# Optimization experiments

Measured on AMD Instinct MI355X. Metric: run time of the kernel, lower is better.

Reference implementation:

```python
import jax, jax.numpy as jnp
import numpy as np

B, H, S, DK = 4, 16, 1024, 64


def setup_inputs() -> dict:
    key = jax.random.key(0)
    kq, kk, kv, km = jax.random.split(key, 4)
    q = jax.random.normal(kq, (B, H, S, DK), dtype=jnp.float32)
    k = jax.random.normal(kk, (B, H, S, DK), dtype=jnp.float32)
    v = jax.random.normal(kv, (B, H, S, DK), dtype=jnp.float32)
    mask = jax.random.randint(km, (B, 1, 1, S), 0, 2).astype(jnp.int32)
    return {"q": q, "k": k, "v": v, "mask": mask}


def reference(q, k, v, mask):
    dk = q.shape[-1]
    scale = 1.0 / np.sqrt(dk).astype(np.float32)
    # [B,H,S,S] scores
    qk = jnp.einsum("bhqd,bhkd->bhqk", q, k) * scale
    qk = jnp.where(mask == 0, jnp.float32(-10000.0), qk)
    attn_weight = jax.nn.softmax(qk, axis=-1)
    # NOTE: faithful to source bug — uses raw masked scores qk, not attn_weight
    output = jnp.einsum("bhqk,bhkd->bhqd", qk, v)
    return (output, attn_weight)
```

## Files before the change

kernel.cpp:

```cpp
#include <hip/hip_runtime.h>


typedef __attribute__((ext_vector_type(4))) float floatx4;
typedef __attribute__((ext_vector_type(8))) short shortx8;
typedef __attribute__((ext_vector_type(8))) unsigned short ushortx8;
typedef __attribute__((ext_vector_type(4))) int intx4;

#define S_ 1024
#define D_ 64
#define NELEM_ 4194304
#define ATTN_OFF 4194304
#define SCN 1040

__device__ __forceinline__ unsigned short f32_to_bf16(float f) {
    union { float f; unsigned u; } a; a.f = f;
    unsigned u = a.u;
    u += 0x7fffu + ((u >> 16) & 1u);
    return (unsigned short)(u >> 16);
}

__device__ __forceinline__ float bf16_to_f32(unsigned short h) {
    union { unsigned u; float f; } a; a.u = ((unsigned)h) << 16;
    return a.f;
}

__device__ __forceinline__ ushortx8 pack8u(floatx4 a, floatx4 b) {
    ushortx8 r;
    r[0] = f32_to_bf16(a[0]); r[1] = f32_to_bf16(a[1]);
    r[2] = f32_to_bf16(a[2]); r[3] = f32_to_bf16(a[3]);
    r[4] = f32_to_bf16(b[0]); r[5] = f32_to_bf16(b[1]);
    r[6] = f32_to_bf16(b[2]); r[7] = f32_to_bf16(b[3]);
    return r;
}

__global__ __launch_bounds__(256) void pack_kv(const float* __restrict__ k,
                                               const float* __restrict__ v,
                                               unsigned short* __restrict__ kbt,
                                               unsigned short* __restrict__ vtp) {
    __shared__ float tile[64][65];
    if (blockIdx.x < 1024) {
        int g = blockIdx.x * 256 + threadIdx.x;
        int lane = g & 63;
        int kt   = (g >> 6) & 63;
        int bh   = g >> 12;
        int quad = lane >> 4;
        int l15  = lane & 15;
        const float* src = k + ((size_t)(bh * S_ + kt * 16 + l15)) * D_ + quad * 8;
        floatx4 f0 = *(const floatx4*)(src);
        floatx4 f1 = *(const floatx4*)(src + 4);
        floatx4 f2 = *(const floatx4*)(src + 32);
        floatx4 f3 = *(const floatx4*)(src + 36);
        unsigned short* dst = kbt + (size_t)g * 16;
        *(ushortx8*)(dst)     = pack8u(f0, f1);
        *(ushortx8*)(dst + 8) = pack8u(f2, f3);
    } else {
        int blk = blockIdx.x - 1024;
        int bh = blk >> 4;
        int s0 = (blk & 15) << 6;
        int tid = threadIdx.x;
        int r  = tid >> 2;
        int c0 = (tid & 3) << 4;
        const float* src = v + ((size_t)(bh * S_ + s0 + r)) * D_ + c0;
        #pragma unroll
        for (int j = 0; j < 4; ++j) {
            floatx4 f = *(const floatx4*)(src + j * 4);
            tile[r][c0 + j*4 + 0] = f[0];
            tile[r][c0 + j*4 + 1] = f[1];
            tile[r][c0 + j*4 + 2] = f[2];
            tile[r][c0 + j*4 + 3] = f[3];
        }
        __syncthreads();
        int d  = tid >> 2;
        int so = (tid & 3) << 4;
        int dt  = d >> 4;
        int l15 = d & 15;
        ushortx8 h0, h1;
        #pragma unroll
        for (int j = 0; j < 8; ++j) h0[j] = f32_to_bf16(tile[so + j][d]);
        #pragma unroll
        for (int j = 0; j < 8; ++j) h1[j] = f32_to_bf16(tile[so + 8 + j][d]);
        int sA = s0 + so;
        int ksA = sA >> 5, qA = (sA & 31) >> 3;
        int sB = sA + 8;
        int ksB = sB >> 5, qB = (sB & 31) >> 3;
        size_t baseA = ((((size_t)bh * 4 + dt) * 32 + ksA) * 64 + qA * 16 + l15) * 8;
        size_t baseB = ((((size_t)bh * 4 + dt) * 32 + ksB) * 64 + qB * 16 + l15) * 8;
        *(ushortx8*)(vtp + baseA) = h0;
        *(ushortx8*)(vtp + baseB) = h1;
    }
}

__global__ __launch_bounds__(256, 4) void attn_main(
    const float* __restrict__ q,
    const int* __restrict__ mask,
    const unsigned short* __restrict__ KbT,
    const unsigned short* __restrict__ VtP,
    float* __restrict__ out)
{
    __shared__ unsigned short sc[16 * SCN];
    __shared__ int msk[1024];

    int g   = blockIdx.x;
    int xcd = g & 7;
    int i   = g >> 3;
    int bh  = xcd * 8 + (i >> 6);
    int q0  = (i & 63) << 4;
    int b   = bh >> 4;
    int tid = threadIdx.x;

    ((intx4*)msk)[tid] = ((const intx4*)(mask + (b << 10)))[tid];

    int w    = tid >> 6;
    int lane = tid & 63;
    int l15  = lane & 15;
    int quad = lane >> 4;

    shortx8 qf0, qf1;
    {
        const float* qb = q + ((size_t)(bh * S_ + q0 + l15)) * D_ + quad * 8;
        floatx4 a0 = *(const floatx4*)(qb);
        floatx4 a1 = *(const floatx4*)(qb + 4);
        floatx4 b0 = *(const floatx4*)(qb + 32);
        floatx4 b1 = *(const floatx4*)(qb + 36);
        ushortx8 u0 = pack8u(a0, a1);
        ushortx8 u1 = pack8u(b0, b1);
        qf0 = (shortx8)u0;
        qf1 = (shortx8)u1;
    }

    __syncthreads();

    {
        const unsigned short* kb = KbT + ((size_t)bh * 64 * 64 + lane) * 16;
        for (int kt = w; kt < 64; kt += 4) {
            const unsigned short* p = kb + (size_t)kt * (64 * 16);
            shortx8 kf0 = *(const shortx8*)(p);
            shortx8 kf1 = *(const shortx8*)(p + 8);
            floatx4 acc = {0.f, 0.f, 0.f, 0.f};
            acc = __builtin_amdgcn_mfma_f32_16x16x32_bf16(qf0, kf0, acc, 0, 0, 0);
            acc = __builtin_amdgcn_mfma_f32_16x16x32_bf16(qf1, kf1, acc, 0, 0, 0);
            int n0 = kt << 4;
            int mv = msk[n0 + l15];
            int col = n0 + l15;
            #pragma unroll
            for (int r = 0; r < 4; ++r) {
                unsigned short h = mv ? f32_to_bf16(acc[r] * 0.125f)
                                      : (unsigned short)0xC61C;
                sc[(quad * 4 + r) * SCN + col] = h;
            }
        }
    }
    __syncthreads();

    {
        float* attnb = out + ATTN_OFF + ((size_t)(bh * S_ + q0)) * S_;
        for (int rr = 0; rr < 4; ++rr) {
            int row = (w << 2) + rr;
            const unsigned short* srow = sc + row * SCN;
            float vv[16];
            #pragma unroll
            for (int c = 0; c < 2; ++c) {
                ushortx8 h = *(const ushortx8*)(srow + (c << 9) + lane * 8);
                #pragma unroll
                for (int j = 0; j < 8; ++j) vv[c * 8 + j] = bf16_to_f32(h[j]);
            }
            float m = vv[0];
            #pragma unroll
            for (int j = 1; j < 16; ++j) m = fmaxf(m, vv[j]);
            #pragma unroll
            for (int off = 32; off; off >>= 1) m = fmaxf(m, __shfl_xor(m, off));
            float s = 0.f;
            #pragma unroll
            for (int j = 0; j < 16; ++j) { vv[j] = __expf(vv[j] - m); s += vv[j]; }
            #pragma unroll
            for (int off = 32; off; off >>= 1) s += __shfl_xor(s, off);
            float inv = 1.0f / s;
            float* arow = attnb + (size_t)row * S_ + lane * 8;
            #pragma unroll
            for (int c = 0; c < 2; ++c) {
                floatx4 o0 = { vv[c*8+0]*inv, vv[c*8+1]*inv, vv[c*8+2]*inv, vv[c*8+3]*inv };
                floatx4 o1 = { vv[c*8+4]*inv, vv[c*8+5]*inv, vv[c*8+6]*inv, vv[c*8+7]*inv };
                *(floatx4*)(arow + (c << 9))     = o0;
                *(floatx4*)(arow + (c << 9) + 4) = o1;
            }
        }
    }

    {
        const unsigned short* vb = VtP + (((size_t)bh * 4 + w) * 32) * (64 * 8) + lane * 8;
        const unsigned short* sr = sc + l15 * SCN + quad * 8;
        floatx4 oacc = {0.f, 0.f, 0.f, 0.f};
        #pragma unroll 4
        for (int ks = 0; ks < 32; ++ks) {
            shortx8 af = *(const shortx8*)(sr + (ks << 5));
            shortx8 bf = *(const shortx8*)(vb + (ks << 9));
            oacc = __builtin_amdgcn_mfma_f32_16x16x32_bf16(af, bf, oacc, 0, 0, 0);
        }
        int d0 = w << 4;
        float* ob = out + ((size_t)(bh * S_ + q0 + (quad << 2))) * D_ + d0 + l15;
        #pragma unroll
        for (int r = 0; r < 4; ++r) ob[(size_t)r * D_] = oacc[r];
    }
}

extern "C" void kernel_launch(void* const* d_in, const int* in_sizes, int n_in,
                              void* d_out, int out_size, void* d_ws, size_t ws_size,
                              hipStream_t stream) {
    const float* q   = (const float*)d_in[0];
    const float* k   = (const float*)d_in[1];
    const float* v   = (const float*)d_in[2];
    const int* mask  = (const int*)d_in[3];
    float* out = (float*)d_out;
    unsigned short* KbT = (unsigned short*)d_ws;
    unsigned short* VtP = KbT + NELEM_;
    pack_kv<<<2048, 256, 0, stream>>>(k, v, KbT, VtP);
    attn_main<<<4096, 256, 0, stream>>>(q, mask, KbT, VtP, out);
}
```

Before: 378.3 us.

## Use 1024-thread blocks over 64 query rows with 2D wave split

Each block now covers 64 query rows with 16 waves split into 4 row groups and 4 column groups. This reuses K and V tiles across more rows per block and cuts the grid to 1024 blocks. Odd waves run the PV matmul before the softmax write-out and even waves do the reverse, so MFMA and store traffic overlap. The cost is about 133 KB of LDS per block and the removal of the XCD-aware block swizzle, which limits blocks per CU and may hurt L2 locality.

```diff
diff --git a/kernel.cpp b/kernel.cpp
--- a/kernel.cpp
+++ b/kernel.cpp
@@ -90,34 +90,34 @@
     }
 }
 
-__global__ __launch_bounds__(256, 4) void attn_main(
+__global__ __launch_bounds__(1024, 4) void attn_main(
     const float* __restrict__ q,
     const int* __restrict__ mask,
     const unsigned short* __restrict__ KbT,
     const unsigned short* __restrict__ VtP,
     float* __restrict__ out)
 {
-    __shared__ unsigned short sc[16 * SCN];
+    __shared__ unsigned short sc[64 * SCN];
     __shared__ int msk[1024];
 
-    int g   = blockIdx.x;
-    int xcd = g & 7;
-    int i   = g >> 3;
-    int bh  = xcd * 8 + (i >> 6);
-    int q0  = (i & 63) << 4;
+    int blk = blockIdx.x;
+    int bh  = blk >> 4;
+    int q0  = (blk & 15) << 6;
     int b   = bh >> 4;
     int tid = threadIdx.x;
 
-    ((intx4*)msk)[tid] = ((const intx4*)(mask + (b << 10)))[tid];
+    msk[tid] = mask[(b << 10) + tid];
 
     int w    = tid >> 6;
     int lane = tid & 63;
     int l15  = lane & 15;
     int quad = lane >> 4;
+    int rg   = w & 3;
+    int cg   = w >> 2;
 
     shortx8 qf0, qf1;
     {
-        const float* qb = q + ((size_t)(bh * S_ + q0 + l15)) * D_ + quad * 8;
+        const float* qb = q + ((size_t)(bh * S_ + q0 + rg * 16 + l15)) * D_ + quad * 8;
         floatx4 a0 = *(const floatx4*)(qb);
         floatx4 a1 = *(const floatx4*)(qb + 4);
         floatx4 b0 = *(const floatx4*)(qb + 32);
@@ -132,7 +132,9 @@
 
     {
         const unsigned short* kb = KbT + ((size_t)bh * 64 * 64 + lane) * 16;
-        for (int kt = w; kt < 64; kt += 4) {
+        #pragma unroll 4
+        for (int t = 0; t < 16; ++t) {
+            int kt = (cg << 4) + t;
             const unsigned short* p = kb + (size_t)kt * (64 * 16);
             shortx8 kf0 = *(const shortx8*)(p);
             shortx8 kf1 = *(const shortx8*)(p + 8);
@@ -146,13 +148,13 @@
             for (int r = 0; r < 4; ++r) {
                 unsigned short h = mv ? f32_to_bf16(acc[r] * 0.125f)
                                       : (unsigned short)0xC61C;
-                sc[(quad * 4 + r) * SCN + col] = h;
+                sc[(rg * 16 + quad * 4 + r) * SCN + col] = h;
             }
         }
     }
     __syncthreads();
 
-    {
+    auto phase2 = [&]() {
         float* attnb = out + ATTN_OFF + ((size_t)(bh * S_ + q0)) * S_;
         for (int rr = 0; rr < 4; ++rr) {
             int row = (w << 2) + rr;
@@ -184,11 +186,10 @@
                 *(floatx4*)(arow + (c << 9) + 4) = o1;
             }
         }
-    }
-
-    {
-        const unsigned short* vb = VtP + (((size_t)bh * 4 + w) * 32) * (64 * 8) + lane * 8;
-        const unsigned short* sr = sc + l15 * SCN + quad * 8;
+    };
+    auto phase3 = [&]() {
+        const unsigned short* vb = VtP + (((size_t)bh * 4 + cg) * 32) * (64 * 8) + lane * 8;
+        const unsigned short* sr = sc + (rg * 16 + l15) * SCN + quad * 8;
         floatx4 oacc = {0.f, 0.f, 0.f, 0.f};
         #pragma unroll 4
         for (int ks = 0; ks < 32; ++ks) {
@@ -196,11 +197,13 @@
             shortx8 bf = *(const shortx8*)(vb + (ks << 9));
             oacc = __builtin_amdgcn_mfma_f32_16x16x32_bf16(af, bf, oacc, 0, 0, 0);
         }
-        int d0 = w << 4;
-        float* ob = out + ((size_t)(bh * S_ + q0 + (quad << 2))) * D_ + d0 + l15;
+        float* ob = out + ((size_t)(bh * S_ + q0 + rg * 16 + (quad << 2))) * D_
+                        + (cg << 4) + l15;
         #pragma unroll
         for (int r = 0; r < 4; ++r) ob[(size_t)r * D_] = oacc[r];
-    }
+    };
+    if (w & 1) { phase3(); phase2(); }
+    else       { phase2(); phase3(); }
 }
 
 extern "C" void kernel_launch(void* const* d_in, const int* in_sizes, int n_in,
@@ -214,5 +217,5 @@
     unsigned short* KbT = (unsigned short*)d_ws;
     unsigned short* VtP = KbT + NELEM_;
     pack_kv<<<2048, 256, 0, stream>>>(k, v, KbT, VtP);
-    attn_main<<<4096, 256, 0, stream>>>(q, mask, KbT, VtP, out);
-}
+    attn_main<<<1024, 1024, 0, stream>>>(q, mask, KbT, VtP, out);
+}
```

Result: faster. 369.8 us (-2.2%).
